# Kernel optimization log

Measured on AMD Instinct MI355X. Metric: run time of the kernel, lower is better.

## Reference

```python
import jax, jax.numpy as jnp
import numpy as np

NUM_CQ = 16
NUM_CODES = 8192
NUM_SAMPLES = 16
TEMP = 1.0
NHEADS = 4
DM = 32
EMB = 768
B, L = 64, 512


def setup_inputs():
    key = jax.random.key(0)
    ks = jax.random.split(key, 16)

    def lin(k, shape):
        fan_in = shape[-1]
        return (jax.random.uniform(k, shape, jnp.float32, -1.0, 1.0) / np.sqrt(fan_in)).astype(jnp.float32)

    xcq = jax.random.normal(ks[0], (B, L, EMB), jnp.float32)
    attn_mask = jax.random.randint(ks[1], (B, L - NUM_CQ), 0, 2, dtype=jnp.int32)
    cb = jax.random.normal(ks[2], (NUM_CODES, EMB), jnp.float32)
    codebook = 100.0 * cb / jnp.linalg.norm(cb, axis=-1, keepdims=True)  # matches 100*normalize init
    return dict(
        xcq=xcq, attn_mask=attn_mask,
        fc_in_w=lin(ks[3], (DM, EMB)), fc_in_b=jnp.zeros((DM,), jnp.float32),
        fc_out_w=lin(ks[4], (EMB, DM)), fc_out_b=jnp.zeros((EMB,), jnp.float32),
        enc_in_w=lin(ks[5], (2, 3 * DM, DM)), enc_in_b=jnp.zeros((2, 3 * DM), jnp.float32),
        enc_out_w=lin(ks[6], (2, DM, DM)), enc_out_b=jnp.zeros((2, DM), jnp.float32),
        enc_ff1_w=lin(ks[7], (2, 2 * DM, DM)), enc_ff1_b=jnp.zeros((2, 2 * DM), jnp.float32),
        enc_ff2_w=lin(ks[8], (2, DM, 2 * DM)), enc_ff2_b=jnp.zeros((2, DM), jnp.float32),
        enc_ln1_g=jnp.ones((2, DM), jnp.float32), enc_ln1_b=jnp.zeros((2, DM), jnp.float32),
        enc_ln2_g=jnp.ones((2, DM), jnp.float32), enc_ln2_b=jnp.zeros((2, DM), jnp.float32),
        codebook=codebook,
    )


def _layernorm(x, g, b):
    mu = jnp.mean(x, -1, keepdims=True)
    var = jnp.mean((x - mu) ** 2, -1, keepdims=True)
    return g * (x - mu) / jnp.sqrt(var + 1e-5) + b


def _forward(xcq, attn_mask, fc_in_w, fc_in_b, fc_out_w, fc_out_b,
             enc_in_w, enc_in_b, enc_out_w, enc_out_b,
             enc_ff1_w, enc_ff1_b, enc_ff2_w, enc_ff2_b,
             enc_ln1_g, enc_ln1_b, enc_ln2_g, enc_ln2_b, codebook):
    Bb, Ll, _ = xcq.shape
    dh = DM // NHEADS
    x = xcq @ fc_in_w.T + fc_in_b  # [B, L, 32]
    # ones for the cq tokens, then the provided mask; True = valid key
    valid = jnp.concatenate([jnp.ones((Bb, NUM_CQ), bool), attn_mask.astype(bool)], axis=1)  # [B, L]
    for l in range(2):  # torch post-norm TransformerEncoderLayer, relu, dropout=0 (eval)
        qkv = x @ enc_in_w[l].T + enc_in_b[l]
        q, k, v = jnp.split(qkv, 3, axis=-1)
        sh = lambda t: t.reshape(Bb, Ll, NHEADS, dh).transpose(0, 2, 1, 3)  # [B,h,L,dh]
        q, k, v = sh(q), sh(k), sh(v)
        scores = jnp.einsum('bhqd,bhkd->bhqk', q, k) / np.sqrt(dh)
        scores = jnp.where(valid[:, None, None, :], scores, -1e9)  # key padding mask
        attn = jax.nn.softmax(scores, axis=-1)
        o = jnp.einsum('bhqk,bhkd->bhqd', attn, v).transpose(0, 2, 1, 3).reshape(Bb, Ll, DM)
        o = o @ enc_out_w[l].T + enc_out_b[l]
        x = _layernorm(x + o, enc_ln1_g[l], enc_ln1_b[l])
        h = jax.nn.relu(x @ enc_ff1_w[l].T + enc_ff1_b[l]) @ enc_ff2_w[l].T + enc_ff2_b[l]
        x = _layernorm(x + h, enc_ln2_g[l], enc_ln2_b[l])
    xc_out = x[:, :NUM_CQ] @ fc_out_w.T + fc_out_b  # [B, ncq, 768]
    flat = xc_out.reshape(-1, EMB)  # [N, 768]
    dists = (jnp.sum(flat ** 2, 1, keepdims=True) + jnp.sum(codebook ** 2, 1)
             - 2.0 * (flat @ codebook.T))  # [N, K] squared euclidean
    logits = (-dists - 1e-5) / TEMP
    N = Bb * NUM_CQ
    # multinomial(total_count=NUM_SAMPLES): draw S categoricals per row and count
    draws = jax.random.categorical(jax.random.key(42), logits, shape=(NUM_SAMPLES, N))  # [S, N]
    rows = jnp.broadcast_to(jnp.arange(N), (NUM_SAMPLES, N))
    samples = jnp.zeros((N, NUM_CODES), jnp.float32).at[rows, draws].add(1.0)  # [N, K] counts
    xq = (samples @ codebook).reshape(xc_out.shape) / NUM_SAMPLES
    xc_quantized = xc_out + jax.lax.stop_gradient(xq - xc_out)  # straight-through estimator
    return xc_quantized


def reference(xcq, attn_mask, fc_in_w, fc_in_b, fc_out_w, fc_out_b,
              enc_in_w, enc_in_b, enc_out_w, enc_out_b,
              enc_ff1_w, enc_ff1_b, enc_ff2_w, enc_ff2_b,
              enc_ln1_g, enc_ln1_b, enc_ln2_g, enc_ln2_b, codebook):
    xc_quantized = _forward(xcq, attn_mask, fc_in_w, fc_in_b, fc_out_w, fc_out_b,
                            enc_in_w, enc_in_b, enc_out_w, enc_out_b,
                            enc_ff1_w, enc_ff1_b, enc_ff2_w, enc_ff2_b,
                            enc_ln1_g, enc_ln1_b, enc_ln2_g, enc_ln2_b, codebook)
    return (xc_quantized, xcq)
```

## Files before the change

### kernel.cpp

```cpp
#include <hip/hip_runtime.h>
#include <stdint.h>

#define NCODES 8192
#define NROWS 1024

#define OFF_LOGITS 0ll
#define OFF_X      8388608ll
#define OFF_QKV    9437184ll
#define OFF_ATTN   12582912ll
#define OFF_FLAT   13631488ll
#define OFF_CSQ    14418944ll

__device__ __forceinline__ uint32_t rotl32(uint32_t x, int r) { return (x << r) | (x >> (32 - r)); }

__device__ __forceinline__ void tf2x32_key42(uint32_t x0, uint32_t x1, uint32_t& o0, uint32_t& o1) {
  const uint32_t k0 = 0u, k1 = 42u;
  const uint32_t k2 = k0 ^ k1 ^ 0x1BD11BDAu;
  x0 += k0; x1 += k1;
  x0 += x1; x1 = rotl32(x1,13); x1 ^= x0;
  x0 += x1; x1 = rotl32(x1,15); x1 ^= x0;
  x0 += x1; x1 = rotl32(x1,26); x1 ^= x0;
  x0 += x1; x1 = rotl32(x1, 6); x1 ^= x0;
  x0 += k1; x1 += k2 + 1u;
  x0 += x1; x1 = rotl32(x1,17); x1 ^= x0;
  x0 += x1; x1 = rotl32(x1,29); x1 ^= x0;
  x0 += x1; x1 = rotl32(x1,16); x1 ^= x0;
  x0 += x1; x1 = rotl32(x1,24); x1 ^= x0;
  x0 += k2; x1 += k0 + 2u;
  x0 += x1; x1 = rotl32(x1,13); x1 ^= x0;
  x0 += x1; x1 = rotl32(x1,15); x1 ^= x0;
  x0 += x1; x1 = rotl32(x1,26); x1 ^= x0;
  x0 += x1; x1 = rotl32(x1, 6); x1 ^= x0;
  x0 += k0; x1 += k1 + 3u;
  x0 += x1; x1 = rotl32(x1,17); x1 ^= x0;
  x0 += x1; x1 = rotl32(x1,29); x1 ^= x0;
  x0 += x1; x1 = rotl32(x1,16); x1 ^= x0;
  x0 += x1; x1 = rotl32(x1,24); x1 ^= x0;
  x0 += k1; x1 += k2 + 4u;
  x0 += x1; x1 = rotl32(x1,13); x1 ^= x0;
  x0 += x1; x1 = rotl32(x1,15); x1 ^= x0;
  x0 += x1; x1 = rotl32(x1,26); x1 ^= x0;
  x0 += x1; x1 = rotl32(x1, 6); x1 ^= x0;
  x0 += k2; x1 += k0 + 5u;
  o0 = x0; o1 = x1;
}

__device__ __forceinline__ float gumbel_at(uint32_t idx) {
  uint32_t y0, y1;
  tf2x32_key42(0u, idx, y0, y1);
  uint32_t bits = y0 ^ y1;
  float f = __uint_as_float((bits >> 9) | 0x3f800000u) - 1.0f;
  float u = fmaxf(f, 1.17549435e-38f);
  return -logf(-logf(u));
}

__global__ __launch_bounds__(256) void k_fcin(const float* __restrict__ xcq,
                                              const float* __restrict__ W,
                                              const float* __restrict__ b,
                                              float* __restrict__ x,
                                              float* __restrict__ outcopy) {
  __shared__ float xs[64 * 36];
  int t = threadIdx.x;
  int w = t >> 6, lane = t & 63;
  long tb = (long)blockIdx.x * 64;
  const float4* xcq4 = (const float4*)xcq;
  float4* out4 = (float4*)outcopy;
  const float4* W4 = (const float4*)W;
  float acc[8];
  #pragma unroll
  for (int i = 0; i < 8; i++) acc[i] = 0.f;

  for (int jc4 = 0; jc4 < 192; jc4 += 8) {
    __syncthreads();
    #pragma unroll
    for (int p = 0; p < 2; p++) {
      int f = t + 256 * p;
      int row = f >> 3, j4 = f & 7;
      long g = (tb + row) * 192 + jc4 + j4;
      float4 v = xcq4[g];
      *(float4*)(xs + row * 36 + j4 * 4) = v;
      out4[g] = v;
    }
    __syncthreads();
    #pragma unroll
    for (int j4 = 0; j4 < 8; j4++) {
      float4 xv = *(const float4*)(xs + lane * 36 + j4 * 4);
      #pragma unroll
      for (int ci = 0; ci < 8; ci++) {
        int c = w * 8 + ci;
        float4 wv = W4[c * 192 + jc4 + j4];
        acc[ci] += xv.x * wv.x + xv.y * wv.y + xv.z * wv.z + xv.w * wv.w;
      }
    }
  }
  __syncthreads();
  *(float4*)(xs + lane * 36 + w * 8)     = make_float4(acc[0] + b[w*8+0], acc[1] + b[w*8+1], acc[2] + b[w*8+2], acc[3] + b[w*8+3]);
  *(float4*)(xs + lane * 36 + w * 8 + 4) = make_float4(acc[4] + b[w*8+4], acc[5] + b[w*8+5], acc[6] + b[w*8+6], acc[7] + b[w*8+7]);
  __syncthreads();
  float4* x4 = (float4*)x;
  #pragma unroll
  for (int p = 0; p < 2; p++) {
    int f = t + 256 * p;
    int row = f >> 3, c4 = f & 7;
    x4[(tb + row) * 8 + c4] = *(const float4*)(xs + row * 36 + c4 * 4);
  }
}

__global__ __launch_bounds__(64) void k_qkv(const float* __restrict__ x,
                                            const float* __restrict__ W,
                                            const float* __restrict__ b,
                                            float* __restrict__ qkv) {
  long token = (long)blockIdx.x * 64 + threadIdx.x;
  const float4* x4 = (const float4*)x;
  const float4* W4 = (const float4*)W;
  float4* q4 = (float4*)qkv;
  float4 xr[8];
  #pragma unroll
  for (int j4 = 0; j4 < 8; j4++) xr[j4] = x4[token * 8 + j4];
  #pragma unroll
  for (int c4 = 0; c4 < 24; c4++) {
    float s[4];
    #pragma unroll
    for (int q = 0; q < 4; q++) {
      int c = c4 * 4 + q;
      float acc = 0.f;
      #pragma unroll
      for (int j4 = 0; j4 < 8; j4++) {
        float4 wv = W4[c * 8 + j4];
        acc += xr[j4].x * wv.x + xr[j4].y * wv.y + xr[j4].z * wv.z + xr[j4].w * wv.w;
      }
      s[q] = acc + b[c];
    }
    q4[token * 24 + c4] = make_float4(s[0], s[1], s[2], s[3]);
  }
}

__global__ __launch_bounds__(256) void k_attn(const float* __restrict__ qkv,
                                              const int* __restrict__ amask,
                                              float* __restrict__ attno) {
  int z = blockIdx.x;
  int b = z >> 3;
  int h = (z >> 1) & 3;
  int half = z & 1;
  __shared__ float4 ks4[512 * 2];
  __shared__ float4 vs4[512 * 2];
  __shared__ float inval[512];
  int t = threadIdx.x;
  long qb4 = (long)b * 512 * 24;
  const float4* qkv4 = (const float4*)qkv;
  #pragma unroll
  for (int p = 0; p < 4; p++) {
    int f = t + 256 * p;
    int tok = f >> 1, hf = f & 1;
    ks4[f] = qkv4[qb4 + (long)tok * 24 + 8 + h * 2 + hf];
    vs4[f] = qkv4[qb4 + (long)tok * 24 + 16 + h * 2 + hf];
  }
  #pragma unroll
  for (int p = 0; p < 2; p++) {
    int l = t + 256 * p;
    inval[l] = (l < 16 || amask[b * 496 + (l - 16)] != 0) ? 0.f : 1.f;
  }
  __syncthreads();
  const float scale = 0.35355339059327373f;
  int lq = half * 256 + t;
  float4 qa = qkv4[qb4 + (long)lq * 24 + h * 2];
  float4 qb = qkv4[qb4 + (long)lq * 24 + h * 2 + 1];
  float m = -3.4e38f;
  for (int lk = 0; lk < 512; lk++) {
    float4 ka = ks4[lk * 2], kb = ks4[lk * 2 + 1];
    float s = qa.x*ka.x + qa.y*ka.y + qa.z*ka.z + qa.w*ka.w
            + qb.x*kb.x + qb.y*kb.y + qb.z*kb.z + qb.w*kb.w;
    s *= scale;
    s = inval[lk] != 0.f ? -1e9f : s;
    m = fmaxf(m, s);
  }
  float denom = 0.f;
  float4 o0 = make_float4(0,0,0,0), o1 = make_float4(0,0,0,0);
  for (int lk = 0; lk < 512; lk++) {
    float4 ka = ks4[lk * 2], kb = ks4[lk * 2 + 1];
    float s = qa.x*ka.x + qa.y*ka.y + qa.z*ka.z + qa.w*ka.w
            + qb.x*kb.x + qb.y*kb.y + qb.z*kb.z + qb.w*kb.w;
    s *= scale;
    s = inval[lk] != 0.f ? -1e9f : s;
    float p = expf(s - m);
    denom += p;
    float4 va = vs4[lk * 2], vb = vs4[lk * 2 + 1];
    o0.x += p * va.x; o0.y += p * va.y; o0.z += p * va.z; o0.w += p * va.w;
    o1.x += p * vb.x; o1.y += p * vb.y; o1.z += p * vb.z; o1.w += p * vb.w;
  }
  float inv = 1.f / denom;
  float4* a4 = (float4*)attno;
  long ob = ((long)b * 512 + lq) * 8 + h * 2;
  a4[ob]     = make_float4(o0.x*inv, o0.y*inv, o0.z*inv, o0.w*inv);
  a4[ob + 1] = make_float4(o1.x*inv, o1.y*inv, o1.z*inv, o1.w*inv);
}

__global__ __launch_bounds__(64) void k_oproj_ln(const float* __restrict__ attno,
                                                 const float* __restrict__ W,
                                                 const float* __restrict__ b,
                                                 const float* __restrict__ g,
                                                 const float* __restrict__ beta,
                                                 float* __restrict__ x) {
  long token = (long)blockIdx.x * 64 + threadIdx.x;
  const float4* a4 = (const float4*)attno;
  const float4* x4 = (const float4*)x;
  const float4* W4 = (const float4*)W;
  float4 orow[8];
  float xr[32];
  #pragma unroll
  for (int j4 = 0; j4 < 8; j4++) {
    orow[j4] = a4[token * 8 + j4];
    float4 v = x4[token * 8 + j4];
    xr[j4*4] = v.x; xr[j4*4+1] = v.y; xr[j4*4+2] = v.z; xr[j4*4+3] = v.w;
  }
  float v[32];
  #pragma unroll
  for (int c = 0; c < 32; c++) {
    float acc = 0.f;
    #pragma unroll
    for (int j4 = 0; j4 < 8; j4++) {
      float4 wv = W4[c * 8 + j4];
      acc += orow[j4].x * wv.x + orow[j4].y * wv.y + orow[j4].z * wv.z + orow[j4].w * wv.w;
    }
    v[c] = acc + b[c] + xr[c];
  }
  float mu = 0.f;
  #pragma unroll
  for (int c = 0; c < 32; c++) mu += v[c];
  mu *= 0.03125f;
  float var = 0.f;
  #pragma unroll
  for (int c = 0; c < 32; c++) { float d = v[c] - mu; var += d * d; }
  var *= 0.03125f;
  float inv = 1.f / sqrtf(var + 1e-5f);
  float4* xo4 = (float4*)x;
  #pragma unroll
  for (int j4 = 0; j4 < 8; j4++) {
    float4 o;
    o.x = g[j4*4]   * (v[j4*4]   - mu) * inv + beta[j4*4];
    o.y = g[j4*4+1] * (v[j4*4+1] - mu) * inv + beta[j4*4+1];
    o.z = g[j4*4+2] * (v[j4*4+2] - mu) * inv + beta[j4*4+2];
    o.w = g[j4*4+3] * (v[j4*4+3] - mu) * inv + beta[j4*4+3];
    xo4[token * 8 + j4] = o;
  }
}

__global__ __launch_bounds__(64) void k_ffn_ln(const float* __restrict__ x,
                                               const float* __restrict__ W1,
                                               const float* __restrict__ b1,
                                               const float* __restrict__ W2,
                                               const float* __restrict__ b2,
                                               const float* __restrict__ g,
                                               const float* __restrict__ beta,
                                               float* __restrict__ xout) {
  long token = (long)blockIdx.x * 64 + threadIdx.x;
  const float4* x4 = (const float4*)x;
  const float4* W14 = (const float4*)W1;
  const float4* W24 = (const float4*)W2;
  float xr[32];
  #pragma unroll
  for (int j4 = 0; j4 < 8; j4++) {
    float4 v = x4[token * 8 + j4];
    xr[j4*4] = v.x; xr[j4*4+1] = v.y; xr[j4*4+2] = v.z; xr[j4*4+3] = v.w;
  }
  float h[64];
  #pragma unroll
  for (int c = 0; c < 64; c++) {
    float acc = 0.f;
    #pragma unroll
    for (int j4 = 0; j4 < 8; j4++) {
      float4 wv = W14[c * 8 + j4];
      acc += xr[j4*4] * wv.x + xr[j4*4+1] * wv.y + xr[j4*4+2] * wv.z + xr[j4*4+3] * wv.w;
    }
    h[c] = fmaxf(acc + b1[c], 0.f);
  }
  float v[32];
  #pragma unroll
  for (int c = 0; c < 32; c++) {
    float acc = 0.f;
    #pragma unroll
    for (int j4 = 0; j4 < 16; j4++) {
      float4 wv = W24[c * 16 + j4];
      acc += h[j4*4] * wv.x + h[j4*4+1] * wv.y + h[j4*4+2] * wv.z + h[j4*4+3] * wv.w;
    }
    v[c] = acc + b2[c] + xr[c];
  }
  float mu = 0.f;
  #pragma unroll
  for (int c = 0; c < 32; c++) mu += v[c];
  mu *= 0.03125f;
  float var = 0.f;
  #pragma unroll
  for (int c = 0; c < 32; c++) { float d = v[c] - mu; var += d * d; }
  var *= 0.03125f;
  float inv = 1.f / sqrtf(var + 1e-5f);
  float4* xo4 = (float4*)xout;
  #pragma unroll
  for (int j4 = 0; j4 < 8; j4++) {
    float4 o;
    o.x = g[j4*4]   * (v[j4*4]   - mu) * inv + beta[j4*4];
    o.y = g[j4*4+1] * (v[j4*4+1] - mu) * inv + beta[j4*4+1];
    o.z = g[j4*4+2] * (v[j4*4+2] - mu) * inv + beta[j4*4+2];
    o.w = g[j4*4+3] * (v[j4*4+3] - mu) * inv + beta[j4*4+3];
    xo4[token * 8 + j4] = o;
  }
}

__global__ __launch_bounds__(256) void k_fcout(const float* __restrict__ x,
                                               const float* __restrict__ W,
                                               const float* __restrict__ b,
                                               float* __restrict__ flat) {
  int bb = blockIdx.x;
  __shared__ float xs[16 * 32];
  int t = threadIdx.x;
  if (t < 128) {
    int row = t >> 3, j4 = t & 7;
    *(float4*)(xs + row * 32 + j4 * 4) =
        *(const float4*)(x + ((long)bb * 512 + row) * 32 + j4 * 4);
  }
  __syncthreads();
  #pragma unroll
  for (int i = 0; i < 3; i++) {
    int e = t + 256 * i;
    const float4* w4 = (const float4*)(W + e * 32);
    float4 wv[8];
    #pragma unroll
    for (int j4 = 0; j4 < 8; j4++) wv[j4] = w4[j4];
    float bias = b[e];
    #pragma unroll
    for (int r = 0; r < 16; r++) {
      float s = 0.f;
      #pragma unroll
      for (int j4 = 0; j4 < 8; j4++) {
        const float* xr = xs + r * 32 + j4 * 4;
        s += xr[0] * wv[j4].x + xr[1] * wv[j4].y + xr[2] * wv[j4].z + xr[3] * wv[j4].w;
      }
      flat[((long)bb * 16 + r) * 768 + e] = s + bias;
    }
  }
}

__global__ __launch_bounds__(256) void k_cbsq(const float* __restrict__ cb,
                                              float* __restrict__ cb_sq) {
  int w = threadIdx.x >> 6, lane = threadIdx.x & 63;
  int k = blockIdx.x * 4 + w;
  const float* row = cb + (long)k * 768;
  float s = 0.f;
  #pragma unroll
  for (int i = 0; i < 12; i++) { float v = row[lane + 64 * i]; s += v * v; }
  #pragma unroll
  for (int off = 32; off >= 1; off >>= 1) s += __shfl_xor(s, off);
  if (lane == 0) cb_sq[k] = s;
}

__global__ __launch_bounds__(256, 2) void k_logits(const float* __restrict__ flat,
                                                   const float* __restrict__ cb,
                                                   const float* __restrict__ cb_sq,
                                                   float* __restrict__ logits) {
  int rb = blockIdx.x >> 5;
  int cblk = blockIdx.x & 31;
  __shared__ float fs[64 * 36];
  __shared__ float cs[256 * 36];
  int t = threadIdx.x;
  int r0 = (t >> 5) * 8;
  int c0 = t & 31;
  long frow = (long)rb * 64;
  long cbase = (long)cblk * 256;
  float acc[8][8];
  #pragma unroll
  for (int ri = 0; ri < 8; ri++)
    #pragma unroll
    for (int ci = 0; ci < 8; ci++) acc[ri][ci] = 0.f;

  for (int kc = 0; kc < 768; kc += 32) {
    __syncthreads();
    #pragma unroll
    for (int p = 0; p < 2; p++) {
      int f = t + 256 * p;
      int row = f >> 3, k4 = f & 7;
      *(float4*)(fs + row * 36 + k4 * 4) =
          *(const float4*)(flat + (frow + row) * 768 + kc + k4 * 4);
    }
    #pragma unroll
    for (int p = 0; p < 8; p++) {
      int col = p * 32 + (t >> 3), k4 = t & 7;
      *(float4*)(cs + col * 36 + k4 * 4) =
          *(const float4*)(cb + (cbase + col) * 768 + kc + k4 * 4);
    }
    __syncthreads();
    #pragma unroll
    for (int k4 = 0; k4 < 8; k4++) {
      float4 fa[8], fb[8];
      #pragma unroll
      for (int i = 0; i < 8; i++) fa[i] = *(const float4*)(fs + (r0 + i) * 36 + k4 * 4);
      #pragma unroll
      for (int i = 0; i < 8; i++) fb[i] = *(const float4*)(cs + (c0 + 32 * i) * 36 + k4 * 4);
      #pragma unroll
      for (int ri = 0; ri < 8; ri++) {
        #pragma unroll
        for (int ci = 0; ci < 8; ci++) {
          acc[ri][ci] = fmaf(fa[ri].x, fb[ci].x, acc[ri][ci]);
          acc[ri][ci] = fmaf(fa[ri].y, fb[ci].y, acc[ri][ci]);
          acc[ri][ci] = fmaf(fa[ri].z, fb[ci].z, acc[ri][ci]);
          acc[ri][ci] = fmaf(fa[ri].w, fb[ci].w, acc[ri][ci]);
        }
      }
    }
  }
  #pragma unroll
  for (int ci = 0; ci < 8; ci++) {
    long col = cbase + c0 + 32 * ci;
    float csq = cb_sq[col];
    #pragma unroll
    for (int ri = 0; ri < 8; ri++) {
      long n = frow + r0 + ri;
      logits[n * 8192 + col] = 2.f * acc[ri][ci] - csq - 1e-5f;
    }
  }
}

__global__ __launch_bounds__(256) void k_sample(const float* __restrict__ logits,
                                                const float* __restrict__ cb,
                                                const float* __restrict__ flat,
                                                float* __restrict__ out0) {
  int n = blockIdx.x, t = threadIdx.x;
  const float* lrow = logits + (long)n * 8192;
  __shared__ float s_max[4];
  __shared__ int s_cnt;
  __shared__ int cand[8192];
  __shared__ float redv[64];
  __shared__ int redi[64];
  __shared__ int draws[16];
  float m = -3.4e38f;
  for (int i = 0; i < 32; i++) m = fmaxf(m, lrow[t + 256 * i]);
  #pragma unroll
  for (int off = 32; off >= 1; off >>= 1) m = fmaxf(m, __shfl_xor(m, off));
  if ((t & 63) == 0) s_max[t >> 6] = m;
  if (t == 0) s_cnt = 0;
  __syncthreads();
  float rowmax = fmaxf(fmaxf(s_max[0], s_max[1]), fmaxf(s_max[2], s_max[3]));
  float thresh = rowmax - 20.5f;
  for (int i = 0; i < 32; i++) {
    int k = t + 256 * i;
    if (lrow[k] >= thresh) { int p = atomicAdd(&s_cnt, 1); cand[p] = k; }
  }
  __syncthreads();
  int ncand = s_cnt;
  float bv[16]; int bi[16];
  #pragma unroll
  for (int s = 0; s < 16; s++) { bv[s] = -3.4e38f; bi[s] = 0x7fffffff; }
  for (int c = t; c < ncand; c += 256) {
    int k = cand[c];
    float lg = lrow[k];
    #pragma unroll
    for (int s = 0; s < 16; s++) {
      uint32_t idx = ((uint32_t)((s << 10) + n) << 13) | (uint32_t)k;
      float val = gumbel_at(idx) + lg;
      if (val > bv[s] || (val == bv[s] && k < bi[s])) { bv[s] = val; bi[s] = k; }
    }
  }
  #pragma unroll
  for (int s = 0; s < 16; s++) {
    #pragma unroll
    for (int off = 32; off >= 1; off >>= 1) {
      float ov = __shfl_xor(bv[s], off);
      int oi = __shfl_xor(bi[s], off);
      if (ov > bv[s] || (ov == bv[s] && oi < bi[s])) { bv[s] = ov; bi[s] = oi; }
    }
    if ((t & 63) == 0) { redv[s * 4 + (t >> 6)] = bv[s]; redi[s * 4 + (t >> 6)] = bi[s]; }
  }
  __syncthreads();
  if (t < 16) {
    float bvv = redv[t * 4]; int bii = redi[t * 4];
    #pragma unroll
    for (int w = 1; w < 4; w++) {
      float ov = redv[t * 4 + w]; int oi = redi[t * 4 + w];
      if (ov > bvv || (ov == bvv && oi < bii)) { bvv = ov; bii = oi; }
    }
    draws[t] = bii;
  }
  __syncthreads();
  #pragma unroll
  for (int i = 0; i < 3; i++) {
    int e = t + 256 * i;
    float ssum = 0.f;
    #pragma unroll
    for (int s = 0; s < 16; s++) ssum += cb[(long)draws[s] * 768 + e];
    float xq = ssum * 0.0625f;
    float fl = flat[(long)n * 768 + e];
    out0[(long)n * 768 + e] = fl + (xq - fl);
  }
}

extern "C" void kernel_launch(void* const* d_in, const int* in_sizes, int n_in,
                              void* d_out, int out_size, void* d_ws, size_t ws_size,
                              hipStream_t stream) {
  (void)in_sizes; (void)n_in; (void)out_size; (void)ws_size;
  const float* xcq      = (const float*)d_in[0];
  const int*   amask    = (const int*)d_in[1];
  const float* fc_in_w  = (const float*)d_in[2];
  const float* fc_in_b  = (const float*)d_in[3];
  const float* fc_out_w = (const float*)d_in[4];
  const float* fc_out_b = (const float*)d_in[5];
  const float* enc_in_w = (const float*)d_in[6];
  const float* enc_in_b = (const float*)d_in[7];
  const float* enc_out_w= (const float*)d_in[8];
  const float* enc_out_b= (const float*)d_in[9];
  const float* ff1w     = (const float*)d_in[10];
  const float* ff1b     = (const float*)d_in[11];
  const float* ff2w     = (const float*)d_in[12];
  const float* ff2b     = (const float*)d_in[13];
  const float* ln1g     = (const float*)d_in[14];
  const float* ln1b     = (const float*)d_in[15];
  const float* ln2g     = (const float*)d_in[16];
  const float* ln2b     = (const float*)d_in[17];
  const float* cb       = (const float*)d_in[18];
  float* out = (float*)d_out;
  float* ws  = (float*)d_ws;

  float* x      = ws + OFF_X;
  float* qkv    = ws + OFF_QKV;
  float* attno  = ws + OFF_ATTN;
  float* flat   = ws + OFF_FLAT;
  float* csq    = ws + OFF_CSQ;
  float* logits = ws + OFF_LOGITS;

  k_fcin<<<512, 256, 0, stream>>>(xcq, fc_in_w, fc_in_b, x, out + 786432);
  for (int l = 0; l < 2; l++) {
    k_qkv<<<512, 64, 0, stream>>>(x, enc_in_w + l * 96 * 32, enc_in_b + l * 96, qkv);
    k_attn<<<512, 256, 0, stream>>>(qkv, amask, attno);
    k_oproj_ln<<<512, 64, 0, stream>>>(attno, enc_out_w + l * 32 * 32, enc_out_b + l * 32,
                                       ln1g + l * 32, ln1b + l * 32, x);
    k_ffn_ln<<<512, 64, 0, stream>>>(x, ff1w + l * 64 * 32, ff1b + l * 64,
                                     ff2w + l * 32 * 64, ff2b + l * 32,
                                     ln2g + l * 32, ln2b + l * 32, x);
  }
  k_fcout<<<64, 256, 0, stream>>>(x, fc_out_w, fc_out_b, flat);
  k_cbsq<<<2048, 256, 0, stream>>>(cb, csq);
  k_logits<<<512, 256, 0, stream>>>(flat, cb, csq, logits);
  k_sample<<<1024, 256, 0, stream>>>(logits, cb, flat, out);
}
```

Measured before the change: 1.110 ms.

## Fuse out-proj and FFN layernorms, prefetch logits tiles, drop attn LDS staging

```diff
diff --git a/kernel.cpp b/kernel.cpp
--- a/kernel.cpp
+++ b/kernel.cpp
@@ -106,11 +106,11 @@
   }
 }
 
-__global__ __launch_bounds__(64) void k_qkv(const float* __restrict__ x,
-                                            const float* __restrict__ W,
-                                            const float* __restrict__ b,
-                                            float* __restrict__ qkv) {
-  long token = (long)blockIdx.x * 64 + threadIdx.x;
+__global__ __launch_bounds__(256) void k_qkv(const float* __restrict__ x,
+                                             const float* __restrict__ W,
+                                             const float* __restrict__ b,
+                                             float* __restrict__ qkv) {
+  long token = (long)blockIdx.x * 256 + threadIdx.x;
   const float4* x4 = (const float4*)x;
   const float4* W4 = (const float4*)W;
   float4* q4 = (float4*)qkv;
@@ -139,52 +139,45 @@
                                               const int* __restrict__ amask,
                                               float* __restrict__ attno) {
   int z = blockIdx.x;
-  int b = z >> 3;
-  int h = (z >> 1) & 3;
-  int half = z & 1;
-  __shared__ float4 ks4[512 * 2];
-  __shared__ float4 vs4[512 * 2];
-  __shared__ float inval[512];
+  int b = z >> 3, h = (z >> 1) & 3, half = z & 1;
   int t = threadIdx.x;
-  long qb4 = (long)b * 512 * 24;
-  const float4* qkv4 = (const float4*)qkv;
-  #pragma unroll
-  for (int p = 0; p < 4; p++) {
-    int f = t + 256 * p;
-    int tok = f >> 1, hf = f & 1;
-    ks4[f] = qkv4[qb4 + (long)tok * 24 + 8 + h * 2 + hf];
-    vs4[f] = qkv4[qb4 + (long)tok * 24 + 16 + h * 2 + hf];
-  }
-  #pragma unroll
-  for (int p = 0; p < 2; p++) {
-    int l = t + 256 * p;
-    inval[l] = (l < 16 || amask[b * 496 + (l - 16)] != 0) ? 0.f : 1.f;
-  }
-  __syncthreads();
+  int lq = half * 256 + t;
+  const float* base = qkv + (long)b * 512 * 96;
+  const float* kbase = base + 32 + h * 8;
+  const float* vbase = base + 64 + h * 8;
+  const int* mrow = amask + b * 496;
+  float4 qa = *(const float4*)(base + (long)lq * 96 + h * 8);
+  float4 qb = *(const float4*)(base + (long)lq * 96 + h * 8 + 4);
   const float scale = 0.35355339059327373f;
-  int lq = half * 256 + t;
-  float4 qa = qkv4[qb4 + (long)lq * 24 + h * 2];
-  float4 qb = qkv4[qb4 + (long)lq * 24 + h * 2 + 1];
   float m = -3.4e38f;
+  #pragma unroll 4
   for (int lk = 0; lk < 512; lk++) {
-    float4 ka = ks4[lk * 2], kb = ks4[lk * 2 + 1];
+    float4 ka = *(const float4*)(kbase + (long)lk * 96);
+    float4 kb = *(const float4*)(kbase + (long)lk * 96 + 4);
     float s = qa.x*ka.x + qa.y*ka.y + qa.z*ka.z + qa.w*ka.w
             + qb.x*kb.x + qb.y*kb.y + qb.z*kb.z + qb.w*kb.w;
     s *= scale;
-    s = inval[lk] != 0.f ? -1e9f : s;
+    int mi = lk - 16 < 0 ? 0 : lk - 16;
+    bool inv = (lk >= 16) && (mrow[mi] == 0);
+    s = inv ? -1e9f : s;
     m = fmaxf(m, s);
   }
   float denom = 0.f;
   float4 o0 = make_float4(0,0,0,0), o1 = make_float4(0,0,0,0);
+  #pragma unroll 4
   for (int lk = 0; lk < 512; lk++) {
-    float4 ka = ks4[lk * 2], kb = ks4[lk * 2 + 1];
+    float4 ka = *(const float4*)(kbase + (long)lk * 96);
+    float4 kb = *(const float4*)(kbase + (long)lk * 96 + 4);
     float s = qa.x*ka.x + qa.y*ka.y + qa.z*ka.z + qa.w*ka.w
             + qb.x*kb.x + qb.y*kb.y + qb.z*kb.z + qb.w*kb.w;
     s *= scale;
-    s = inval[lk] != 0.f ? -1e9f : s;
+    int mi = lk - 16 < 0 ? 0 : lk - 16;
+    bool inv = (lk >= 16) && (mrow[mi] == 0);
+    s = inv ? -1e9f : s;
     float p = expf(s - m);
     denom += p;
-    float4 va = vs4[lk * 2], vb = vs4[lk * 2 + 1];
+    float4 va = *(const float4*)(vbase + (long)lk * 96);
+    float4 vb = *(const float4*)(vbase + (long)lk * 96 + 4);
     o0.x += p * va.x; o0.y += p * va.y; o0.z += p * va.z; o0.w += p * va.w;
     o1.x += p * vb.x; o1.y += p * vb.y; o1.z += p * vb.z; o1.w += p * vb.w;
   }
@@ -195,16 +188,19 @@
   a4[ob + 1] = make_float4(o1.x*inv, o1.y*inv, o1.z*inv, o1.w*inv);
 }
 
-__global__ __launch_bounds__(64) void k_oproj_ln(const float* __restrict__ attno,
-                                                 const float* __restrict__ W,
-                                                 const float* __restrict__ b,
-                                                 const float* __restrict__ g,
-                                                 const float* __restrict__ beta,
-                                                 float* __restrict__ x) {
-  long token = (long)blockIdx.x * 64 + threadIdx.x;
+__global__ __launch_bounds__(256) void k_post(const float* __restrict__ attno,
+      float* __restrict__ x,
+      const float* __restrict__ Wo, const float* __restrict__ bo,
+      const float* __restrict__ g1, const float* __restrict__ be1,
+      const float* __restrict__ W1, const float* __restrict__ b1,
+      const float* __restrict__ W2, const float* __restrict__ b2,
+      const float* __restrict__ g2, const float* __restrict__ be2) {
+  long token = (long)blockIdx.x * 256 + threadIdx.x;
   const float4* a4 = (const float4*)attno;
   const float4* x4 = (const float4*)x;
-  const float4* W4 = (const float4*)W;
+  const float4* Wo4 = (const float4*)Wo;
+  const float4* W14 = (const float4*)W1;
+  const float4* W24 = (const float4*)W2;
   float4 orow[8];
   float xr[32];
   #pragma unroll
@@ -219,10 +215,10 @@
     float acc = 0.f;
     #pragma unroll
     for (int j4 = 0; j4 < 8; j4++) {
-      float4 wv = W4[c * 8 + j4];
+      float4 wv = Wo4[c * 8 + j4];
       acc += orow[j4].x * wv.x + orow[j4].y * wv.y + orow[j4].z * wv.z + orow[j4].w * wv.w;
     }
-    v[c] = acc + b[c] + xr[c];
+    v[c] = acc + bo[c] + xr[c];
   }
   float mu = 0.f;
   #pragma unroll
@@ -232,37 +228,11 @@
   #pragma unroll
   for (int c = 0; c < 32; c++) { float d = v[c] - mu; var += d * d; }
   var *= 0.03125f;
-  float inv = 1.f / sqrtf(var + 1e-5f);
-  float4* xo4 = (float4*)x;
-  #pragma unroll
-  for (int j4 = 0; j4 < 8; j4++) {
-    float4 o;
-    o.x = g[j4*4]   * (v[j4*4]   - mu) * inv + beta[j4*4];
-    o.y = g[j4*4+1] * (v[j4*4+1] - mu) * inv + beta[j4*4+1];
-    o.z = g[j4*4+2] * (v[j4*4+2] - mu) * inv + beta[j4*4+2];
-    o.w = g[j4*4+3] * (v[j4*4+3] - mu) * inv + beta[j4*4+3];
-    xo4[token * 8 + j4] = o;
-  }
-}
-
-__global__ __launch_bounds__(64) void k_ffn_ln(const float* __restrict__ x,
-                                               const float* __restrict__ W1,
-                                               const float* __restrict__ b1,
-                                               const float* __restrict__ W2,
-                                               const float* __restrict__ b2,
-                                               const float* __restrict__ g,
-                                               const float* __restrict__ beta,
-                                               float* __restrict__ xout) {
-  long token = (long)blockIdx.x * 64 + threadIdx.x;
-  const float4* x4 = (const float4*)x;
-  const float4* W14 = (const float4*)W1;
-  const float4* W24 = (const float4*)W2;
-  float xr[32];
-  #pragma unroll
-  for (int j4 = 0; j4 < 8; j4++) {
-    float4 v = x4[token * 8 + j4];
-    xr[j4*4] = v.x; xr[j4*4+1] = v.y; xr[j4*4+2] = v.z; xr[j4*4+3] = v.w;
-  }
+  float inv1 = 1.f / sqrtf(var + 1e-5f);
+  float y[32];
+  #pragma unroll
+  for (int c = 0; c < 32; c++) y[c] = g1[c] * (v[c] - mu) * inv1 + be1[c];
+
   float h[64];
   #pragma unroll
   for (int c = 0; c < 64; c++) {
@@ -270,11 +240,11 @@
     #pragma unroll
     for (int j4 = 0; j4 < 8; j4++) {
       float4 wv = W14[c * 8 + j4];
-      acc += xr[j4*4] * wv.x + xr[j4*4+1] * wv.y + xr[j4*4+2] * wv.z + xr[j4*4+3] * wv.w;
+      acc += y[j4*4] * wv.x + y[j4*4+1] * wv.y + y[j4*4+2] * wv.z + y[j4*4+3] * wv.w;
     }
     h[c] = fmaxf(acc + b1[c], 0.f);
   }
-  float v[32];
+  float v2[32];
   #pragma unroll
   for (int c = 0; c < 32; c++) {
     float acc = 0.f;
@@ -283,25 +253,25 @@
       float4 wv = W24[c * 16 + j4];
       acc += h[j4*4] * wv.x + h[j4*4+1] * wv.y + h[j4*4+2] * wv.z + h[j4*4+3] * wv.w;
     }
-    v[c] = acc + b2[c] + xr[c];
-  }
-  float mu = 0.f;
-  #pragma unroll
-  for (int c = 0; c < 32; c++) mu += v[c];
+    v2[c] = acc + b2[c] + y[c];
+  }
+  mu = 0.f;
+  #pragma unroll
+  for (int c = 0; c < 32; c++) mu += v2[c];
   mu *= 0.03125f;
-  float var = 0.f;
-  #pragma unroll
-  for (int c = 0; c < 32; c++) { float d = v[c] - mu; var += d * d; }
+  var = 0.f;
+  #pragma unroll
+  for (int c = 0; c < 32; c++) { float d = v2[c] - mu; var += d * d; }
   var *= 0.03125f;
-  float inv = 1.f / sqrtf(var + 1e-5f);
-  float4* xo4 = (float4*)xout;
+  float inv2 = 1.f / sqrtf(var + 1e-5f);
+  float4* xo4 = (float4*)x;
   #pragma unroll
   for (int j4 = 0; j4 < 8; j4++) {
     float4 o;
-    o.x = g[j4*4]   * (v[j4*4]   - mu) * inv + beta[j4*4];
-    o.y = g[j4*4+1] * (v[j4*4+1] - mu) * inv + beta[j4*4+1];
-    o.z = g[j4*4+2] * (v[j4*4+2] - mu) * inv + beta[j4*4+2];
-    o.w = g[j4*4+3] * (v[j4*4+3] - mu) * inv + beta[j4*4+3];
+    o.x = g2[j4*4]   * (v2[j4*4]   - mu) * inv2 + be2[j4*4];
+    o.y = g2[j4*4+1] * (v2[j4*4+1] - mu) * inv2 + be2[j4*4+1];
+    o.z = g2[j4*4+2] * (v2[j4*4+2] - mu) * inv2 + be2[j4*4+2];
+    o.w = g2[j4*4+3] * (v2[j4*4+3] - mu) * inv2 + be2[j4*4+3];
     xo4[token * 8 + j4] = o;
   }
 }
@@ -353,7 +323,7 @@
   if (lane == 0) cb_sq[k] = s;
 }
 
-__global__ __launch_bounds__(256, 2) void k_logits(const float* __restrict__ flat,
+__global__ __launch_bounds__(256, 3) void k_logits(const float* __restrict__ flat,
                                                    const float* __restrict__ cb,
                                                    const float* __restrict__ cb_sq,
                                                    float* __restrict__ logits) {
@@ -366,6 +336,17 @@
   int c0 = t & 31;
   long frow = (long)rb * 64;
   long cbase = (long)cblk * 256;
+  int ldr = t >> 3, ldk = t & 7;
+
+  const float* fptr = flat + (frow + ldr) * 768 + ldk * 4;
+  const float* cptr = cb + (cbase + ldr) * 768 + ldk * 4;
+
+  float4 pf_f[2], pf_c[8];
+  #pragma unroll
+  for (int p = 0; p < 2; p++) pf_f[p] = *(const float4*)(fptr + (long)(32 * p) * 768);
+  #pragma unroll
+  for (int p = 0; p < 8; p++) pf_c[p] = *(const float4*)(cptr + (long)(32 * p) * 768);
+
   float acc[8][8];
   #pragma unroll
   for (int ri = 0; ri < 8; ri++)
@@ -375,34 +356,34 @@
   for (int kc = 0; kc < 768; kc += 32) {
     __syncthreads();
     #pragma unroll
-    for (int p = 0; p < 2; p++) {
-      int f = t + 256 * p;
-      int row = f >> 3, k4 = f & 7;
-      *(float4*)(fs + row * 36 + k4 * 4) =
-          *(const float4*)(flat + (frow + row) * 768 + kc + k4 * 4);
-    }
-    #pragma unroll
-    for (int p = 0; p < 8; p++) {
-      int col = p * 32 + (t >> 3), k4 = t & 7;
-      *(float4*)(cs + col * 36 + k4 * 4) =
-          *(const float4*)(cb + (cbase + col) * 768 + kc + k4 * 4);
-    }
+    for (int p = 0; p < 2; p++)
+      *(float4*)(fs + (ldr + 32 * p) * 36 + ldk * 4) = pf_f[p];
+    #pragma unroll
+    for (int p = 0; p < 8; p++)
+      *(float4*)(cs + (ldr + 32 * p) * 36 + ldk * 4) = pf_c[p];
     __syncthreads();
+    if (kc + 32 < 768) {
+      #pragma unroll
+      for (int p = 0; p < 2; p++)
+        pf_f[p] = *(const float4*)(fptr + (long)(32 * p) * 768 + kc + 32);
+      #pragma unroll
+      for (int p = 0; p < 8; p++)
+        pf_c[p] = *(const float4*)(cptr + (long)(32 * p) * 768 + kc + 32);
+    }
     #pragma unroll
     for (int k4 = 0; k4 < 8; k4++) {
-      float4 fa[8], fb[8];
-      #pragma unroll
-      for (int i = 0; i < 8; i++) fa[i] = *(const float4*)(fs + (r0 + i) * 36 + k4 * 4);
+      float4 fb[8];
       #pragma unroll
       for (int i = 0; i < 8; i++) fb[i] = *(const float4*)(cs + (c0 + 32 * i) * 36 + k4 * 4);
       #pragma unroll
       for (int ri = 0; ri < 8; ri++) {
+        float4 fa = *(const float4*)(fs + (r0 + ri) * 36 + k4 * 4);
         #pragma unroll
         for (int ci = 0; ci < 8; ci++) {
-          acc[ri][ci] = fmaf(fa[ri].x, fb[ci].x, acc[ri][ci]);
-          acc[ri][ci] = fmaf(fa[ri].y, fb[ci].y, acc[ri][ci]);
-          acc[ri][ci] = fmaf(fa[ri].z, fb[ci].z, acc[ri][ci]);
-          acc[ri][ci] = fmaf(fa[ri].w, fb[ci].w, acc[ri][ci]);
+          acc[ri][ci] = fmaf(fa.x, fb[ci].x, acc[ri][ci]);
+          acc[ri][ci] = fmaf(fa.y, fb[ci].y, acc[ri][ci]);
+          acc[ri][ci] = fmaf(fa.z, fb[ci].z, acc[ri][ci]);
+          acc[ri][ci] = fmaf(fa.w, fb[ci].w, acc[ri][ci]);
         }
       }
     }
@@ -527,13 +508,14 @@
 
   k_fcin<<<512, 256, 0, stream>>>(xcq, fc_in_w, fc_in_b, x, out + 786432);
   for (int l = 0; l < 2; l++) {
-    k_qkv<<<512, 64, 0, stream>>>(x, enc_in_w + l * 96 * 32, enc_in_b + l * 96, qkv);
+    k_qkv<<<128, 256, 0, stream>>>(x, enc_in_w + l * 96 * 32, enc_in_b + l * 96, qkv);
     k_attn<<<512, 256, 0, stream>>>(qkv, amask, attno);
-    k_oproj_ln<<<512, 64, 0, stream>>>(attno, enc_out_w + l * 32 * 32, enc_out_b + l * 32,
-                                       ln1g + l * 32, ln1b + l * 32, x);
-    k_ffn_ln<<<512, 64, 0, stream>>>(x, ff1w + l * 64 * 32, ff1b + l * 64,
-                                     ff2w + l * 32 * 64, ff2b + l * 32,
-                                     ln2g + l * 32, ln2b + l * 32, x);
+    k_post<<<128, 256, 0, stream>>>(attno, x,
+                                    enc_out_w + l * 32 * 32, enc_out_b + l * 32,
+                                    ln1g + l * 32, ln1b + l * 32,
+                                    ff1w + l * 64 * 32, ff1b + l * 64,
+                                    ff2w + l * 32 * 64, ff2b + l * 32,
+                                    ln2g + l * 32, ln2b + l * 32);
   }
   k_fcout<<<64, 256, 0, stream>>>(x, fc_out_w, fc_out_b, flat);
   k_cbsq<<<2048, 256, 0, stream>>>(cb, csq);
```

Measured after the change: 1.727 ms. +55.5%, slower.
